# Kernel optimization log

Hardware: AMD Instinct MI355X
Metric: run time of the kernel (lower is better)

Reference implementation:

```python
import jax, jax.numpy as jnp
import numpy as np

NEURAL_DIM = 512
N_UNITS = 512
N_DAYS = 24
N_CLASSES = 41
N_LAYERS = 5
PATCH = 14
STRIDE = 4
MEMORY_SIZE = 256
IN0 = NEURAL_DIM * PATCH  # 7168, layer-0 input after patch concat


def _expm(M):
    """Matrix exponential via scaling-and-squaring + Taylor (float64 numpy)."""
    nrm = np.linalg.norm(M, 1)
    s = max(0, int(np.ceil(np.log2(nrm))) + 4) if nrm > 0 else 0
    Ms = M / (2.0 ** s)
    n = M.shape[0]
    E = np.eye(n)
    term = np.eye(n)
    for k in range(1, 25):
        term = term @ Ms / k
        E = E + term
    for _ in range(s):
        E = E @ E
    return E


def _lmu_AB(m_size):
    # NOTE: the torch cell calls _compute_A_B(memory_size, B.shape[0]), so the
    # effective theta used for discretization is memory_size itself.
    theta = float(m_size)
    q = np.arange(m_size, dtype=np.float64)
    R = ((2.0 * q + 1.0) / theta).reshape(-1, 1)
    i, j = np.meshgrid(q, q, indexing='ij')
    A = R * np.where(i < j, -1.0, (-1.0) ** (i - j + 1))
    Bc = R * ((-1.0) ** q).reshape(-1, 1)
    # zero-order hold discretization with dt=1: expm([[A,B],[0,0]])
    aug = np.zeros((m_size + 1, m_size + 1))
    aug[:m_size, :m_size] = A
    aug[:m_size, m_size:] = Bc
    E = _expm(aug)
    return (jnp.asarray(E[:m_size, :m_size], dtype=jnp.float32),
            jnp.asarray(E[:m_size, m_size:], dtype=jnp.float32))


A_MAT, B_MAT = _lmu_AB(MEMORY_SIZE)  # [M,M], [M,1]


def setup_inputs() -> dict:
    key = jax.random.key(0)
    ks = jax.random.split(key, 20)

    def rn(k, shape, scale):
        return jax.random.normal(k, shape, dtype=jnp.float32) * scale

    inp = {
        'x': jax.random.normal(ks[0], (32, 1024, NEURAL_DIM), dtype=jnp.float32),
        'day_idx': jax.random.randint(ks[1], (32,), 0, N_DAYS),
        # day-specific input layers (init: identity + zero bias; perturb slightly)
        'day_W': jnp.broadcast_to(jnp.eye(NEURAL_DIM, dtype=jnp.float32), (N_DAYS, NEURAL_DIM, NEURAL_DIM)) + rn(ks[2], (N_DAYS, NEURAL_DIM, NEURAL_DIM), 0.01),
        'day_b': rn(ks[3], (N_DAYS, 1, NEURAL_DIM), 0.01),
        # layer 0 (input 7168)
        'e_x0': rn(ks[4], (1, IN0), 1.0 / np.sqrt(IN0)),
        'W_x0': rn(ks[5], (N_UNITS, IN0), np.sqrt(2.0 / (IN0 + N_UNITS))),
        # layers 1..4 (input 512)
        'e_xr': rn(ks[6], (N_LAYERS - 1, 1, N_UNITS), 1.0 / np.sqrt(N_UNITS)),
        'W_xr': rn(ks[7], (N_LAYERS - 1, N_UNITS, N_UNITS), np.sqrt(1.0 / N_UNITS)),
        # shared-shape per-layer params (stacked over 5 layers)
        'e_h': rn(ks[8], (N_LAYERS, 1, N_UNITS), 1.0 / np.sqrt(N_UNITS)),
        'e_m': rn(ks[9], (N_LAYERS, 1, MEMORY_SIZE), 0.02),
        'W_h': rn(ks[10], (N_LAYERS, N_UNITS, N_UNITS), np.sqrt(1.0 / N_UNITS)),
        'W_m': rn(ks[11], (N_LAYERS, N_UNITS, MEMORY_SIZE), np.sqrt(2.0 / (MEMORY_SIZE + N_UNITS))),
        'h0': rn(ks[12], (N_LAYERS, 1, N_UNITS), 0.05),
        'm0': rn(ks[13], (N_LAYERS, 1, MEMORY_SIZE), 0.05),
        'out_W': rn(ks[14], (N_CLASSES, N_UNITS), np.sqrt(2.0 / (N_UNITS + N_CLASSES))),
        'out_b': jnp.zeros((N_CLASSES,), dtype=jnp.float32),
    }
    return inp


def _run_lmu_layer(seq, e_x, W_x, e_h, e_m, W_h, W_m, h_init, m_init):
    """seq: [B,T,in] -> [B,T,H] LMU recurrence."""
    # precompute input projections (the only big GEMMs) outside the scan
    xWx = jnp.einsum('bti,hi->bth', seq, W_x)   # [B,T,H]
    xex = jnp.einsum('bti,oi->bto', seq, e_x)   # [B,T,1]

    def step(carry, inp):
        h, m = carry
        xw, xe = inp
        u = xe + h @ e_h.T + m @ e_m.T          # [B,1]
        m = m @ A_MAT.T + u @ B_MAT.T           # [B,M]
        h = jnp.tanh(xw + h @ W_h.T + m @ W_m.T)
        return (h, m), h

    (_, _), hs = jax.lax.scan(step, (h_init, m_init),
                              (jnp.swapaxes(xWx, 0, 1), jnp.swapaxes(xex, 0, 1)))
    return jnp.swapaxes(hs, 0, 1)  # [B,T,H]


def reference(x, day_idx, day_W, day_b, e_x0, W_x0, e_xr, W_xr,
              e_h, e_m, W_h, W_m, h0, m0, out_W, out_b):
    B = x.shape[0]
    # day-specific linear + softsign
    h = jnp.einsum('btd,bdk->btk', x, day_W[day_idx]) + day_b[day_idx]
    h = h / (1.0 + jnp.abs(h))  # Softsign
    # patch concat: unfold time dim with window=PATCH, stride=STRIDE
    T = h.shape[1]
    Tp = (T - PATCH) // STRIDE + 1
    idx = jnp.arange(Tp)[:, None] * STRIDE + jnp.arange(PATCH)[None, :]
    h = h[:, idx, :].reshape(B, Tp, PATCH * NEURAL_DIM)  # [B,Tp,7168]

    bc = lambda v, d: jnp.broadcast_to(v, (B, d))
    seq = _run_lmu_layer(h, e_x0, W_x0, e_h[0], e_m[0], W_h[0], W_m[0],
                         bc(h0[0], N_UNITS), bc(m0[0], MEMORY_SIZE))
    for i in range(1, N_LAYERS):
        seq = _run_lmu_layer(seq, e_xr[i - 1], W_xr[i - 1], e_h[i], e_m[i],
                             W_h[i], W_m[i], bc(h0[i], N_UNITS), bc(m0[i], MEMORY_SIZE))
    logits = seq @ out_W.T + out_b  # [B,Tp,n_classes]
    return logits
```

## Files before the change

### kernel.cpp

```cpp
#include <hip/hip_runtime.h>
#include <hip/hip_fp16.h>

typedef _Float16 f16;
typedef _Float16 f16x8 __attribute__((ext_vector_type(8)));
typedef _Float16 f16x4 __attribute__((ext_vector_type(4)));
typedef float f32x4 __attribute__((ext_vector_type(4)));
typedef int int4v __attribute__((ext_vector_type(4)));

#define DI static __device__ __forceinline__

constexpr int N2 = 257 * 257;
#define LSTRIDE ((size_t)254 * 32 * 768)
#define HWREG_XCC_ID 63508
#define FSTRIDE 256

DI f32x4 mfma16(f16x8 a, f16x8 b, f32x4 c) {
  return __builtin_amdgcn_mfma_f32_16x16x32_f16(a, b, c, 0, 0, 0);
}
DI f16x8 ldg8(const f16* p) { return *reinterpret_cast<const f16x8*>(p); }
DI f16x8 cvt8(const float* s) {
  f16x8 v;
#pragma unroll
  for (int j = 0; j < 8; ++j) v[j] = (f16)s[j];
  return v;
}
DI double invfact(int k) {
  double f = 1.0;
  for (int i = 2; i <= k; ++i) f *= (double)i;
  return 1.0 / f;
}

DI void st_d_sc1(double* p, double v) {
  asm volatile("global_store_dwordx2 %0, %1, off sc1" :: "v"(p), "v"(v) : "memory");
}
DI void st_f_sc1(float* p, float v) {
  asm volatile("global_store_dword %0, %1, off sc1" :: "v"(p), "v"(v) : "memory");
}
DI void st_h_sc1(f16* p, f16 v) {
  asm volatile("global_store_short %0, %1, off sc1" :: "v"(p), "v"(v) : "memory");
}
DI void st_b_sc1(unsigned char* p, int v) {
  asm volatile("global_store_byte %0, %1, off sc1" :: "v"(p), "v"(v) : "memory");
}
DI void st8_sc1(f16* p, f16x4 v) {
  asm volatile("global_store_dwordx2 %0, %1, off sc1\n\ts_waitcnt vmcnt(0)"
               :: "v"(p), "v"(v) : "memory");
}
DI void st8_plain(f16* p, f16x4 v) {
  asm volatile("global_store_dwordx2 %0, %1, off\n\ts_waitcnt vmcnt(0)"
               :: "v"(p), "v"(v) : "memory");
}
DI void st8_fast(f16* p, f16x4 v) {
  asm volatile(
      "global_store_dwordx2 %0, %1, off\n\t"
      "global_store_dwordx2 %0, %1, off sc1\n\t"
      "s_waitcnt vmcnt(1)"
      :: "v"(p), "v"(v) : "memory");
}
DI void atomic_bump_l2(int* p) {
  int one = 1;
  asm volatile("global_atomic_add %0, %1, off" :: "v"(p), "v"(one) : "memory");
}
DI int atomic_read_l2(int* p) {
  int v, zero = 0;
  asm volatile("global_atomic_add %0, %1, %2, off sc0\n\ts_waitcnt vmcnt(0)"
               : "=v"(v) : "v"(p), "v"(zero) : "memory");
  return v;
}
DI int ld_llc(const int* p) {
  return __hip_atomic_load(p, __ATOMIC_RELAXED, __HIP_MEMORY_SCOPE_AGENT);
}
DI void add_llc(int* p) {
  __hip_atomic_fetch_add(p, 1, __ATOMIC_RELAXED, __HIP_MEMORY_SCOPE_AGENT);
}
DI int fetchadd_llc(int* p) {
  return __hip_atomic_fetch_add(p, 1, __ATOMIC_RELAXED, __HIP_MEMORY_SCOPE_AGENT);
}
DI void drain_vm() { asm volatile("s_waitcnt vmcnt(0)" ::: "memory"); }
DI void membar() {
  __builtin_amdgcn_sched_barrier(0);
  asm volatile("" ::: "memory");
}
DI bool l16ok(int4v a) {
  return a.x == 0x01010101 && a.y == 0x01010101 && a.z == 0x01010101 && a.w == 0x01010101;
}
DI int4v ld16_sc1(const int* p) {
  int4v b;
  asm volatile("global_load_dwordx4 %0, %1, off sc1\n\ts_waitcnt vmcnt(0)"
               : "=v"(b) : "v"(p) : "memory");
  return b;
}
template <bool HASP>
DI void poll_slow(const int* fl, const int* pl) {
  for (int it = 0; it < (1 << 14); ++it) {
    int4v b, c;
    asm volatile(
        "global_load_dwordx4 %0, %2, off sc1\n\t"
        "global_load_dwordx4 %1, %3, off sc1\n\t"
        "s_waitcnt vmcnt(0)"
        : "=&v"(b), "=&v"(c)
        : "v"(fl), "v"(pl) : "memory");
    bool prv = HASP ? l16ok(c) : true;
    if (l16ok(b) & prv) return;
    __builtin_amdgcn_s_sleep(1);
  }
}
DI float tanh_fast(float x) {
  x = fminf(9.f, fmaxf(-9.f, x));
  float e = __expf(2.f * x);
  return __fdividef(e - 1.f, e + 1.f);
}

DI void gridbar_nf(int* bar, int nwg) {
  drain_vm();
  __syncthreads();
  if (threadIdx.x == 0) {
    int g = ld_llc(bar + 1);
    int old = __hip_atomic_fetch_add(bar, 1, __ATOMIC_RELAXED, __HIP_MEMORY_SCOPE_AGENT);
    if (old == nwg - 1) {
      __hip_atomic_store(bar, 0, __ATOMIC_RELAXED, __HIP_MEMORY_SCOPE_AGENT);
      add_llc(bar + 1);
    } else {
      for (int it = 0; it < (1 << 14) && ld_llc(bar + 1) == g; ++it)
        __builtin_amdgcn_s_sleep(1);
    }
  }
  __syncthreads();
}

DI void mm257(double* __restrict__ D, const double* __restrict__ A, const double* __restrict__ Bm,
              int fj, const double* __restrict__ T1, const double* __restrict__ T2,
              const double* __restrict__ T3, int gtid, int nth) {
  double c0 = 0, c1 = 0, c2 = 0, c3 = 0;
  if (fj >= 0) {
    c0 = invfact(4 * fj); c1 = invfact(4 * fj + 1);
    c2 = invfact(4 * fj + 2); c3 = invfact(4 * fj + 3);
  }
  for (int e = gtid; e < N2; e += nth) {
    int i = e / 257, j = e - i * 257;
    const double* ar = A + (size_t)i * 257;
    const double* bc = Bm + j;
    double s0 = 0, s1 = 0, s2 = 0, s3 = 0;
    for (int k = 0; k < 256; k += 4) {
      s0 = fma(ar[k], bc[(size_t)k * 257], s0);
      s1 = fma(ar[k + 1], bc[(size_t)(k + 1) * 257], s1);
      s2 = fma(ar[k + 2], bc[(size_t)(k + 2) * 257], s2);
      s3 = fma(ar[k + 3], bc[(size_t)(k + 3) * 257], s3);
    }
    double s = ((s0 + s1) + (s2 + s3)) + ar[256] * bc[(size_t)256 * 257];
    if (fj >= 0) s += c0 * ((i == j) ? 1.0 : 0.0) + c1 * T1[e] + c2 * T2[e] + c3 * T3[e];
    st_d_sc1(D + e, s);
  }
}

__global__ __launch_bounds__(256) void k_setup(
    const float* __restrict__ dayW, const float* __restrict__ ex0, const float* __restrict__ Wx0,
    const float* __restrict__ exr, const float* __restrict__ Wxr,
    const float* __restrict__ eh, const float* __restrict__ em,
    const float* __restrict__ Wh, const float* __restrict__ Wm, const float* __restrict__ outW,
    double* __restrict__ X, float* __restrict__ w1f, float* __restrict__ AWt,
    float* __restrict__ btf, f16* __restrict__ gbuf, f16* __restrict__ wxcat,
    f16* __restrict__ outw, f16* __restrict__ dayWt, int* __restrict__ bar) {
  const int gtid = blockIdx.x * 256 + threadIdx.x;
  const int nth = 128 * 256;
  double* Ms = X;
  double* M2 = X + N2;
  double* M3 = X + 2 * N2;
  double* M4 = X + 3 * N2;
  double* H = X + 4 * N2;
  double* S = X + 11 * N2;

  for (int e = gtid; e < N2; e += nth) {
    int i = e / 257, j = e - i * 257;
    double v = 0.0;
    if (i < 256) {
      double R = (2.0 * i + 1.0) / 256.0;
      if (j < 256) v = R * ((i < j) ? -1.0 : (((i - j) & 1) ? 1.0 : -1.0));
      else v = R * ((i & 1) ? -1.0 : 1.0);
    }
    st_d_sc1(Ms + e, v / 64.0);
  }
  for (int e = gtid; e < 576 * 896; e += nth) {
    int n = e / 896, kc = (e - n * 896) * 8;
    f16x8 v;
    if (n < 512) v = cvt8(Wx0 + (size_t)n * 7168 + kc);
    else if (n == 512) v = cvt8(ex0 + kc);
    else {
#pragma unroll
      for (int j = 0; j < 8; ++j) v[j] = (f16)0.f;
    }
    *reinterpret_cast<f16x8*>(wxcat + (size_t)n * 7168 + kc) = v;
  }
  for (int e = gtid; e < 48 * 64; e += nth) {
    int n = e / 64, kc = (e - n * 64) * 8;
    f16x8 v;
    if (n < 41) v = cvt8(outW + (size_t)n * 512 + kc);
    else {
#pragma unroll
      for (int j = 0; j < 8; ++j) v[j] = (f16)0.f;
    }
    *reinterpret_cast<f16x8*>(outw + (size_t)n * 512 + kc) = v;
  }
  {
    __shared__ float tile[64][65];
    for (int tt = blockIdx.x; tt < 24 * 64; tt += 128) {
      int D = tt >> 6; int r = tt & 63; int kb = (r >> 3) * 64; int nb = (r & 7) * 64;
      __syncthreads();
      for (int q = 0; q < 16; ++q) {
        int idx = threadIdx.x + q * 256; int kk = idx >> 6; int nn = idx & 63;
        tile[kk][nn] = dayW[(size_t)D * 262144 + (size_t)(kb + kk) * 512 + nb + nn];
      }
      __syncthreads();
      for (int q = 0; q < 2; ++q) {
        int cidx = threadIdx.x + q * 256; int nn = cidx >> 3; int kc = (cidx & 7) * 8;
        f16x8 v;
#pragma unroll
        for (int jj = 0; jj < 8; ++jj) v[jj] = (f16)tile[kc + jj][nn];
        *reinterpret_cast<f16x8*>(dayWt + (size_t)D * 262144 + (size_t)(nb + nn) * 512 + kb + kc) = v;
      }
    }
    __syncthreads();
  }
  gridbar_nf(bar, 128);

  mm257(M2, Ms, Ms, -1, Ms, Ms, Ms, gtid, nth); gridbar_nf(bar, 128);
  mm257(M3, M2, Ms, -1, Ms, Ms, Ms, gtid, nth); gridbar_nf(bar, 128);
  mm257(M4, M2, M2, -1, Ms, Ms, Ms, gtid, nth);
  for (int e = gtid; e < N2; e += nth) {
    int i = e / 257, j = e - i * 257;
    st_d_sc1(H + e, (i == j) ? invfact(24) : 0.0);
  }
  gridbar_nf(bar, 128);
  for (int k = 0; k < 6; ++k) {
    mm257(H + (size_t)(k + 1) * N2, H + (size_t)k * N2, M4, 5 - k, Ms, M2, M3, gtid, nth);
    gridbar_nf(bar, 128);
  }
  {
    const double* Ssrc = H + (size_t)6 * N2;
    for (int k = 0; k < 6; ++k) {
      mm257(S + (size_t)k * N2, Ssrc, Ssrc, -1, Ms, Ms, Ms, gtid, nth);
      gridbar_nf(bar, 128);
      Ssrc = S + (size_t)k * N2;
    }
  }
  const double* E = S + (size_t)5 * N2;

  for (int e = gtid; e < 256; e += nth) st_f_sc1(btf + e, (float)E[(size_t)e * 257 + 256]);
  for (int e = gtid; e < 5 * 512; e += nth) {
    int l = e / 512, n = e - l * 512;
    const float* wm = Wm + ((size_t)l * 512 + n) * 256;
    float s = 0.f;
    for (int j = 0; j < 256; ++j) s += (float)E[(size_t)j * 257 + 256] * wm[j];
    st_f_sc1(w1f + e, s);
  }
  for (int e = gtid; e < 5 * 512 * 256; e += nth) {
    int l = e / (512 * 256); int r = e - l * 512 * 256; int n = r >> 8; int i = r & 255;
    const double* Ec = E + i;
    const float* wm = Wm + ((size_t)l * 512 + n) * 256;
    float s0 = 0, s1 = 0, s2 = 0, s3 = 0;
    for (int j = 0; j < 256; j += 4) {
      s0 += (float)Ec[(size_t)j * 257] * wm[j];
      s1 += (float)Ec[(size_t)(j + 1) * 257] * wm[j + 1];
      s2 += (float)Ec[(size_t)(j + 2) * 257] * wm[j + 2];
      s3 += (float)Ec[(size_t)(j + 3) * 257] * wm[j + 3];
    }
    st_f_sc1(AWt + e, (s0 + s1) + (s2 + s3));
  }
  gridbar_nf(bar, 128);

  for (int e = gtid; e < 5 * 768 * 160; e += nth) {
    int l = e / (768 * 160); int r = e - l * 768 * 160; int n = r / 160; int k = (r - n * 160) * 8;
    if (l == 0 && k >= 768) continue;
    f16x8 v;
    if (n < 512) {
      float w1n = w1f[l * 512 + n];
      if (k < 512) {
        const float* a = Wh + ((size_t)l * 512 + n) * 512 + k;
        const float* b = eh + (size_t)l * 512 + k;
#pragma unroll
        for (int jj = 0; jj < 8; ++jj) v[jj] = (f16)(a[jj] + b[jj] * w1n);
      } else if (k < 768) {
        int i = k - 512;
        const float* a = AWt + ((size_t)l * 512 + n) * 256 + i;
        const float* b = em + (size_t)l * 256 + i;
#pragma unroll
        for (int jj = 0; jj < 8; ++jj) v[jj] = (f16)(a[jj] + b[jj] * w1n);
      } else {
        int d = k - 768;
        const float* a = Wxr + ((size_t)(l - 1) * 512 + n) * 512 + d;
        const float* b = exr + (size_t)(l - 1) * 512 + d;
#pragma unroll
        for (int jj = 0; jj < 8; ++jj) v[jj] = (f16)(a[jj] + b[jj] * w1n);
      }
    } else {
      int jm = n - 512;
      float btn = btf[jm];
      if (k < 512) {
        const float* b = eh + (size_t)l * 512 + k;
#pragma unroll
        for (int jj = 0; jj < 8; ++jj) v[jj] = (f16)(b[jj] * btn);
      } else if (k < 768) {
        int i = k - 512;
        const double* a = E + (size_t)jm * 257 + i;
        const float* b = em + (size_t)l * 256 + i;
#pragma unroll
        for (int jj = 0; jj < 8; ++jj) v[jj] = (f16)((float)a[jj] + b[jj] * btn);
      } else {
        int d = k - 768;
        const float* b = exr + (size_t)(l - 1) * 512 + d;
#pragma unroll
        for (int jj = 0; jj < 8; ++jj) v[jj] = (f16)(b[jj] * btn);
      }
    }
    *reinterpret_cast<f16x8*>(gbuf + ((size_t)l * 768 + n) * 1280 + k) = v;
  }
}

__global__ __launch_bounds__(256) void k_day(const float* __restrict__ x,
    const int* __restrict__ dayIdx, const float* __restrict__ dayb,
    const f16* __restrict__ dayWt, f16* __restrict__ h1) {
  __shared__ f16 As[64][40];
  __shared__ f16 Bs[256][40];
  const int bid = blockIdx.x;
  const int b = bid >> 5; const int r = bid & 31;
  const int t0 = (r >> 1) * 64; const int n0 = (r & 1) * 256;
  const int D = dayIdx[b];
  const int tid = threadIdx.x, lane = tid & 63, w = tid >> 6, q4 = lane >> 4;
  const float* xb = x + ((size_t)b * 1024 + t0) * 512;
  const f16* Wt = dayWt + (size_t)D * 262144 + (size_t)n0 * 512;
  f32x4 acc[16];
#pragma unroll
  for (int i = 0; i < 16; ++i) acc[i] = (f32x4){0.f, 0.f, 0.f, 0.f};
  for (int kt = 0; kt < 16; ++kt) {
    const int k0 = kt * 32;
    __syncthreads();
    { int row = tid >> 2, c8 = (tid & 3) * 8;
      *reinterpret_cast<f16x8*>(&As[row][c8]) = cvt8(xb + (size_t)row * 512 + k0 + c8); }
    for (int q = 0; q < 4; ++q) {
      int idx = tid + q * 256; int row = idx >> 2; int c8 = (idx & 3) * 8;
      *reinterpret_cast<f16x8*>(&Bs[row][c8]) = ldg8(Wt + (size_t)row * 512 + k0 + c8);
    }
    __syncthreads();
    f16x8 a = *reinterpret_cast<const f16x8*>(&As[w * 16 + (lane & 15)][q4 * 8]);
#pragma unroll
    for (int nt2 = 0; nt2 < 16; ++nt2) {
      f16x8 bb = *reinterpret_cast<const f16x8*>(&Bs[nt2 * 16 + (lane & 15)][q4 * 8]);
      acc[nt2] = mfma16(a, bb, acc[nt2]);
    }
  }
#pragma unroll
  for (int nt2 = 0; nt2 < 16; ++nt2) {
    int n = n0 + nt2 * 16 + (lane & 15);
    float db = dayb[(size_t)D * 512 + n];
#pragma unroll
    for (int i = 0; i < 4; ++i) {
      int t = t0 + w * 16 + q4 * 4 + i;
      float v = acc[nt2][i] + db;
      v = v / (1.f + fabsf(v));
      h1[((size_t)b * 1024 + t) * 512 + n] = (f16)v;
    }
  }
}

__global__ __launch_bounds__(256) void k_xw0(const f16* __restrict__ h1,
    const f16* __restrict__ wxcat, float* __restrict__ xw0) {
  __shared__ f16 As[128][40];
  __shared__ f16 Bs[96][40];
  const int bid = blockIdx.x;
  const int mt = bid / 6; const int nb = bid - mt * 6;
  const int m0 = mt * 128; const int n0 = nb * 96;
  const int tid = threadIdx.x, lane = tid & 63, w = tid >> 6, q4 = lane >> 4;
  f32x4 acc[2][6];
#pragma unroll
  for (int a = 0; a < 2; ++a)
#pragma unroll
    for (int b = 0; b < 6; ++b) acc[a][b] = (f32x4){0.f, 0.f, 0.f, 0.f};
  for (int kt = 0; kt < 224; ++kt) {
    const int k0 = kt * 32; const int p = k0 >> 9; const int kd = k0 & 511;
    __syncthreads();
    for (int q = 0; q < 2; ++q) {
      int idx = tid + q * 256; int row = idx >> 2; int c8 = (idx & 3) * 8;
      int m = m0 + row; int b = m >> 8; int tp = m & 255; if (tp > 252) tp = 252;
      *reinterpret_cast<f16x8*>(&As[row][c8]) =
          ldg8(h1 + ((size_t)b * 1024 + (size_t)tp * 4 + p) * 512 + kd + c8);
    }
    for (int q = 0; q < 2; ++q) {
      int idx = tid + q * 256;
      if (idx < 384) {
        int row = idx >> 2; int c8 = (idx & 3) * 8;
        *reinterpret_cast<f16x8*>(&Bs[row][c8]) =
            ldg8(wxcat + (size_t)(n0 + row) * 7168 + k0 + c8);
      }
    }
    __syncthreads();
#pragma unroll
    for (int mb = 0; mb < 2; ++mb) {
      f16x8 a = *reinterpret_cast<const f16x8*>(&As[w * 32 + mb * 16 + (lane & 15)][q4 * 8]);
#pragma unroll
      for (int nt2 = 0; nt2 < 6; ++nt2) {
        f16x8 bb = *reinterpret_cast<const f16x8*>(&Bs[nt2 * 16 + (lane & 15)][q4 * 8]);
        acc[mb][nt2] = mfma16(a, bb, acc[mb][nt2]);
      }
    }
  }
#pragma unroll
  for (int mb = 0; mb < 2; ++mb)
#pragma unroll
    for (int nt2 = 0; nt2 < 6; ++nt2)
#pragma unroll
      for (int i = 0; i < 4; ++i) {
        int m = m0 + w * 32 + mb * 16 + q4 * 4 + i;
        int n = n0 + nt2 * 16 + (lane & 15);
        xw0[(size_t)m * 576 + n] = acc[mb][nt2][i];
      }
}

template <int KK, bool FAST>
DI void rec_run(int l, int c, int tid, const f16* __restrict__ gbuf, f16* __restrict__ sbuf,
                const float* __restrict__ xw0, const float* __restrict__ w1f,
                const float* __restrict__ btf, const float* __restrict__ h0,
                const float* __restrict__ m0, char* fastL, unsigned char* fastX,
                unsigned char* slowF, f16* bflds, f16* smtile) {
  const int lane = tid & 63, w = tid >> 6;
  const int mb = w / 3, nt = w % 3;
  const int nbase = c * 48 + nt * 16;
  const int ncol = nbase + (lane & 15);
  const int q4 = lane >> 4;

  for (int r = tid; r < 32 * 48; r += 384) {
    int row = r / 48; int col = c * 48 + (r - row * 48);
    float v = (col < 512) ? h0[(size_t)l * 512 + col] : m0[(size_t)l * 256 + col - 512];
    f16* p = sbuf + (size_t)l * LSTRIDE + (size_t)row * 768 + col;
    if (FAST) *p = (f16)v;
    else st_h_sc1(p, (f16)v);
  }

  const f16* gb = gbuf + ((size_t)l * 768 + ncol) * 1280 + (size_t)q4 * 8;
  constexpr int NREG = (KK > 32) ? 32 : KK;
  f16x8 bf[NREG];
#pragma unroll
  for (int kk = 0; kk < NREG; ++kk) bf[kk] = ldg8(gb + (size_t)kk * 32);
  if (KK == 40) {
#pragma unroll
    for (int kk = 32; kk < 40; ++kk) {
      f16x8 v = ldg8(gb + (size_t)kk * 32);
      *reinterpret_cast<f16x8*>(bflds + ((size_t)(w * 8 + (kk - 32)) * 64 + lane) * 8) = v;
    }
  }
  float w1n = 0.f, btn = 0.f;
  if (KK == 24) {
    if (ncol < 512) w1n = w1f[ncol];
    else btn = btf[ncol - 512];
  }
  drain_vm();
  __syncthreads();
  if (tid == 0) {
    if (FAST) {
      atomic_bump_l2((int*)(fastL + (size_t)l * 4096));
      st_b_sc1(fastX + (size_t)(l * 256) * 16 + c, 1);
    } else {
      st_b_sc1(slowF + (size_t)(l * FSTRIDE) * 16 + c, 1);
    }
  }

  int pready = 0;
  int lwin = 64, lfails = 0;

  for (int t = 0; t < 253; ++t) {
    float xadd[4];
    if (KK == 24) {
#pragma unroll
      for (int i = 0; i < 4; ++i) {
        const int brow = mb * 16 + q4 * 4 + i;
        const float* xr = xw0 + ((size_t)brow * 256 + t) * 576;
        float xe = xr[512];
        xadd[i] = (ncol < 512) ? (xr[ncol] + xe * w1n) : (xe * btn);
      }
    }
    if (tid == 0) {
      if (FAST) {
        if (l > 0 && pready <= t) {
          int la = t + 4; if (la > 253) la = 253;
          const int* p1 = (const int*)(fastX + (size_t)((l - 1) * 256 + t + 1) * 16);
          const int* p2 = (const int*)(fastX + (size_t)((l - 1) * 256 + la) * 16);
          for (int it = 0; it < (1 << 14); ++it) {
            int4v a, b;
            asm volatile(
                "global_load_dwordx4 %0, %2, off sc1\n\t"
                "global_load_dwordx4 %1, %3, off sc1\n\t"
                "s_waitcnt vmcnt(0)"
                : "=&v"(a), "=&v"(b) : "v"(p1), "v"(p2) : "memory");
            if (l16ok(b)) { pready = la; break; }
            if (l16ok(a)) { pready = t + 1; break; }
            __builtin_amdgcn_s_sleep(1);
          }
        }
        int* cl = (int*)(fastL + (size_t)l * 4096 + (size_t)t * 16);
        bool got = false;
        for (int it = 0; it < lwin; ++it) {
          if (atomic_read_l2(cl) >= 16) { got = true; break; }
          __builtin_amdgcn_s_sleep(1);
        }
        if (!got) {
          if (++lfails >= 3) lwin = 4;
          const int* fx = (const int*)(fastX + (size_t)(l * 256 + t) * 16);
          for (int j = 0; j < (1 << 14); ++j) {
            if (atomic_read_l2(cl) >= 16) break;
            if (l16ok(ld16_sc1(fx))) break;
            __builtin_amdgcn_s_sleep(1);
          }
        }
      } else {
        const int* fl = (const int*)(slowF + (size_t)(l * FSTRIDE + t) * 16);
        const int* pl = (l > 0) ? (const int*)(slowF + (size_t)((l - 1) * FSTRIDE + t + 1) * 16) : fl;
        if (l > 0) poll_slow<true>(fl, pl);
        else poll_slow<false>(fl, pl);
      }
    }
    __builtin_amdgcn_s_barrier();
    membar();

    const int arow = mb * 16 + (lane & 15);
    const f16* s0 = sbuf + (size_t)l * LSTRIDE + ((size_t)t * 32 + arow) * 768 + (size_t)q4 * 8;
    f32x4 acc = {0.f, 0.f, 0.f, 0.f};
#pragma unroll
    for (int kk = 0; kk < 24; ++kk) acc = mfma16(ldg8(s0 + (size_t)kk * 32), bf[kk < NREG ? kk : 0], acc);
    if (KK == 40) {
      const f16* s1 = sbuf + (size_t)(l - 1) * LSTRIDE + ((size_t)(t + 1) * 32 + arow) * 768 + (size_t)q4 * 8;
#pragma unroll
      for (int kk = 24; kk < 32; ++kk) acc = mfma16(ldg8(s1 + (size_t)(kk - 24) * 32), bf[kk < NREG ? kk : 0], acc);
#pragma unroll
      for (int kk = 32; kk < 40; ++kk) {
        f16x8 bb = *reinterpret_cast<const f16x8*>(bflds + ((size_t)(w * 8 + (kk - 32)) * 64 + lane) * 8);
        acc = mfma16(ldg8(s1 + (size_t)(kk - 24) * 32), bb, acc);
      }
    }

    const int scol = nt * 16 + (lane & 15);
#pragma unroll
    for (int i = 0; i < 4; ++i) {
      float v = acc[i];
      if (KK == 24) v += xadd[i];
      if (ncol < 512) v = tanh_fast(v);
      smtile[(mb * 16 + q4 * 4 + i) * 48 + scol] = (f16)v;
    }
    __syncthreads();
    {
      int row = tid / 12; int c4 = (tid - row * 12) * 4;
      f16x4 v4 = *reinterpret_cast<const f16x4*>(smtile + row * 48 + c4);
      f16* dst = sbuf + (size_t)l * LSTRIDE + ((size_t)(t + 1) * 32 + row) * 768 + c * 48 + c4;
      if (!FAST) st8_sc1(dst, v4);
      else if (l < 4) st8_fast(dst, v4);
      else st8_plain(dst, v4);
    }
    __builtin_amdgcn_s_barrier();
    if (FAST) {
      if (tid == 0) atomic_bump_l2((int*)(fastL + (size_t)l * 4096 + (size_t)(t + 1) * 16));
      if (l < 4) drain_vm();
      __builtin_amdgcn_s_barrier();
      if (tid == 0) st_b_sc1(fastX + (size_t)(l * 256 + t + 1) * 16 + c, 1);
    } else {
      if (tid == 0) st_b_sc1(slowF + (size_t)(l * FSTRIDE + t + 1) * 16 + c, 1);
    }
  }
}

__global__ __launch_bounds__(384, 2) void k_rec(const f16* __restrict__ gbuf, f16* __restrict__ sbuf,
    const float* __restrict__ xw0, const float* __restrict__ w1f,
    const float* __restrict__ btf, const float* __restrict__ h0,
    const float* __restrict__ m0, char* __restrict__ fastL,
    unsigned char* __restrict__ fastX, unsigned char* __restrict__ slowF,
    int* __restrict__ xcdcnt, int* __restrict__ globalcnt, int* __restrict__ verdict) {
  __shared__ f16 bflds[6 * 8 * 64 * 8];
  __shared__ f16 smtile[32 * 48];
  __shared__ int sh[4];

  if (threadIdx.x == 0) {
    unsigned xcd = ((unsigned)__builtin_amdgcn_s_getreg(HWREG_XCC_ID)) & 7u;
    int pt = fetchadd_llc(xcdcnt + xcd);
    drain_vm();
    int gt = fetchadd_llc(globalcnt);
    if (gt == 255) {
      int ok = 1;
      for (int i = 0; i < 5; ++i)
        if (ld_llc(xcdcnt + i) < 16) ok = 0;
      __hip_atomic_store(verdict, ok ? 1 : 2, __ATOMIC_RELAXED, __HIP_MEMORY_SCOPE_AGENT);
    }
    int v = 0;
    for (int it = 0; it < (1 << 17); ++it) {
      v = ld_llc(verdict);
      if (v) break;
      __builtin_amdgcn_s_sleep(4);
    }
    if (v == 0) v = 2;
    int L = -1, C = 0;
    if (v == 1) {
      if (xcd < 5 && pt < 16) { L = (int)xcd; C = pt; }
    } else {
      if (gt < 80) { L = gt >> 4; C = gt & 15; }
    }
    sh[0] = L; sh[1] = C; sh[2] = (L >= 0); sh[3] = (v == 1);
  }
  __syncthreads();
  if (!sh[2]) return;
  const int l = sh[0], c = sh[1];
  const bool fast = (sh[3] != 0);

  if (fast) {
    if (l == 0) rec_run<24, true>(0, c, threadIdx.x, gbuf, sbuf, xw0, w1f, btf, h0, m0, fastL, fastX, slowF, bflds, smtile);
    else        rec_run<40, true>(l, c, threadIdx.x, gbuf, sbuf, xw0, w1f, btf, h0, m0, fastL, fastX, slowF, bflds, smtile);
  } else {
    if (l == 0) rec_run<24, false>(0, c, threadIdx.x, gbuf, sbuf, xw0, w1f, btf, h0, m0, fastL, fastX, slowF, bflds, smtile);
    else        rec_run<40, false>(l, c, threadIdx.x, gbuf, sbuf, xw0, w1f, btf, h0, m0, fastL, fastX, slowF, bflds, smtile);
  }
}

__global__ __launch_bounds__(256) void k_out(const f16* __restrict__ sbuf4,
    const f16* __restrict__ outw, const float* __restrict__ outb, float* __restrict__ out) {
  const int bid = blockIdx.x; const int b = bid >> 2; const int tp0 = (bid & 3) * 64;
  const int tid = threadIdx.x, lane = tid & 63, w = tid >> 6, q4 = lane >> 4;
  f32x4 acc[3];
#pragma unroll
  for (int i = 0; i < 3; ++i) acc[i] = (f32x4){0.f, 0.f, 0.f, 0.f};
  int tq = tp0 + w * 16 + (lane & 15) + 1;
  const int tau = tq > 253 ? 253 : tq;
  const f16* arow = sbuf4 + ((size_t)tau * 32 + b) * 768 + (size_t)q4 * 8;
#pragma unroll
  for (int kk = 0; kk < 16; ++kk) {
    f16x8 a = ldg8(arow + (size_t)kk * 32);
#pragma unroll
    for (int nt2 = 0; nt2 < 3; ++nt2) {
      f16x8 bb = ldg8(outw + (size_t)(nt2 * 16 + (lane & 15)) * 512 + kk * 32 + q4 * 8);
      acc[nt2] = mfma16(a, bb, acc[nt2]);
    }
  }
#pragma unroll
  for (int nt2 = 0; nt2 < 3; ++nt2) {
    int cc = nt2 * 16 + (lane & 15);
    if (cc < 41) {
      float ob = outb[cc];
#pragma unroll
      for (int i = 0; i < 4; ++i) {
        int tp = tp0 + w * 16 + q4 * 4 + i;
        if (tp < 253) out[((size_t)b * 253 + tp) * 41 + cc] = acc[nt2][i] + ob;
      }
    }
  }
}

extern "C" void kernel_launch(void* const* d_in, const int* in_sizes, int n_in,
                              void* d_out, int out_size, void* d_ws, size_t ws_size,
                              hipStream_t stream) {
  const float* x      = (const float*)d_in[0];
  const int*   dayIdx = (const int*)d_in[1];
  const float* day_W  = (const float*)d_in[2];
  const float* day_b  = (const float*)d_in[3];
  const float* e_x0   = (const float*)d_in[4];
  const float* W_x0   = (const float*)d_in[5];
  const float* e_xr   = (const float*)d_in[6];
  const float* W_xr   = (const float*)d_in[7];
  const float* e_h    = (const float*)d_in[8];
  const float* e_m    = (const float*)d_in[9];
  const float* W_h    = (const float*)d_in[10];
  const float* W_m    = (const float*)d_in[11];
  const float* h0     = (const float*)d_in[12];
  const float* m0     = (const float*)d_in[13];
  const float* out_W  = (const float*)d_in[14];
  const float* out_b  = (const float*)d_in[15];
  float* outp = (float*)d_out;

  char* w = (char*)d_ws;
  size_t o = 0;
  auto al = [&](size_t n) { void* p = w + o; o = (o + n + 255) & ~(size_t)255; return p; };

  char*  flags = (char*) al(65536);
  f16*   gbuf  = (f16*)  al((size_t)5 * 768 * 1280 * 2);
  f16*   outw  = (f16*)  al((size_t)48 * 512 * 2);
  float* xw0   = (float*)al((size_t)8192 * 576 * 4);
  float* w1f   = (float*)al((size_t)5 * 512 * 4);
  float* btf   = (float*)al(256 * 4);

  const size_t XB    = ((size_t)17 * N2 * 8 + 255) & ~(size_t)255;
  const size_t AWTB  = ((size_t)5 * 512 * 256 * 4 + 255) & ~(size_t)255;
  const size_t DAYB  = ((size_t)24 * 512 * 512 * 2 + 255) & ~(size_t)255;
  const size_t WXB   = ((size_t)576 * 7168 * 2 + 255) & ~(size_t)255;
  const size_t H1B   = ((size_t)32 * 1024 * 512 * 2 + 255) & ~(size_t)255;
  const size_t SBUFB = (size_t)5 * LSTRIDE * 2;
  size_t ovb = XB + AWTB + DAYB + WXB + H1B;
  if (SBUFB > ovb) ovb = SBUFB;
  char* ov = (char*)al(ovb);
  double* X     = (double*)ov;
  float*  AWt   = (float*)(ov + XB);
  f16*    dayWt = (f16*)(ov + XB + AWTB);
  f16*    wxcat = (f16*)(ov + XB + AWTB + DAYB);
  f16*    h1    = (f16*)(ov + XB + AWTB + DAYB + WXB);
  f16*    sbuf  = (f16*)ov;

  if (o > ws_size) return;
  (void)in_sizes; (void)n_in; (void)out_size;

  hipMemsetAsync(flags, 0, 65536, stream);
  k_setup<<<128, 256, 0, stream>>>(day_W, e_x0, W_x0, e_xr, W_xr, e_h, e_m, W_h, W_m,
                                   out_W, X, w1f, AWt, btf, gbuf, wxcat, outw, dayWt,
                                   (int*)(flags + 61504));
  k_day<<<1024, 256, 0, stream>>>(x, dayIdx, day_b, dayWt, h1);
  k_xw0<<<384, 256, 0, stream>>>(h1, wxcat, xw0);
  k_rec<<<256, 384, 0, stream>>>(gbuf, sbuf, xw0, w1f, btf, h0, m0,
                                 flags, (unsigned char*)(flags + 20480),
                                 (unsigned char*)(flags + 40960),
                                 (int*)(flags + 61440), (int*)(flags + 61472),
                                 (int*)(flags + 61476));
  k_out<<<128, 256, 0, stream>>>(sbuf + (size_t)4 * LSTRIDE, outw, out_b, outp);
}
```

Before: 4.166 ms.

## Add per-XCD byte flag array for fast-path step sync and block mm257 by four columns

Adds a new fastP byte-flag array that each producer block writes with a plain store, and consumers poll it with a 16-byte sc0 load instead of reading an L2 atomic counter. The atomic counter and the sc1 flags stay as fallbacks. This aims to cut the latency of the per-timestep cross-block handoff in the recurrent kernel. It also restructures the setup matrix multiply so each thread computes four adjacent output columns, reusing each A element for four FMAs. The flag region grows and its offsets move. There is a risk that plain and sc0 accesses may not be coherent across XCDs, which would make the fallback path run more often.

New measurement: 5.812 ms. 39.5% more time.

```diff
diff --git a/kernel.cpp b/kernel.cpp
--- a/kernel.cpp
+++ b/kernel.cpp
@@ -38,6 +38,9 @@
 }
 DI void st_h_sc1(f16* p, f16 v) {
   asm volatile("global_store_short %0, %1, off sc1" :: "v"(p), "v"(v) : "memory");
+}
+DI void st_b_plain(unsigned char* p, int v) {
+  asm volatile("global_store_byte %0, %1, off" :: "v"(p), "v"(v) : "memory");
 }
 DI void st_b_sc1(unsigned char* p, int v) {
   asm volatile("global_store_byte %0, %1, off sc1" :: "v"(p), "v"(v) : "memory");
@@ -83,6 +86,12 @@
 }
 DI bool l16ok(int4v a) {
   return a.x == 0x01010101 && a.y == 0x01010101 && a.z == 0x01010101 && a.w == 0x01010101;
+}
+DI int4v ld16_sc0(const int* p) {
+  int4v b;
+  asm volatile("global_load_dwordx4 %0, %1, off sc0\n\ts_waitcnt vmcnt(0)"
+               : "=v"(b) : "v"(p) : "memory");
+  return b;
 }
 DI int4v ld16_sc1(const int* p) {
   int4v b;
@@ -136,20 +145,36 @@
     c0 = invfact(4 * fj); c1 = invfact(4 * fj + 1);
     c2 = invfact(4 * fj + 2); c3 = invfact(4 * fj + 3);
   }
-  for (int e = gtid; e < N2; e += nth) {
-    int i = e / 257, j = e - i * 257;
+  const int NB = 257 * 65;
+  for (int e = gtid; e < NB; e += nth) {
+    int i = e / 65, jb = e - i * 65;
+    int j0 = jb * 4;
     const double* ar = A + (size_t)i * 257;
-    const double* bc = Bm + j;
-    double s0 = 0, s1 = 0, s2 = 0, s3 = 0;
-    for (int k = 0; k < 256; k += 4) {
-      s0 = fma(ar[k], bc[(size_t)k * 257], s0);
-      s1 = fma(ar[k + 1], bc[(size_t)(k + 1) * 257], s1);
-      s2 = fma(ar[k + 2], bc[(size_t)(k + 2) * 257], s2);
-      s3 = fma(ar[k + 3], bc[(size_t)(k + 3) * 257], s3);
-    }
-    double s = ((s0 + s1) + (s2 + s3)) + ar[256] * bc[(size_t)256 * 257];
-    if (fj >= 0) s += c0 * ((i == j) ? 1.0 : 0.0) + c1 * T1[e] + c2 * T2[e] + c3 * T3[e];
-    st_d_sc1(D + e, s);
+    if (j0 < 256) {
+      const double* bc = Bm + j0;
+      double s0 = 0, s1 = 0, s2 = 0, s3 = 0;
+      for (int k = 0; k < 257; ++k) {
+        double a = ar[k];
+        const double* br = bc + (size_t)k * 257;
+        s0 = fma(a, br[0], s0); s1 = fma(a, br[1], s1);
+        s2 = fma(a, br[2], s2); s3 = fma(a, br[3], s3);
+      }
+      double sv[4] = {s0, s1, s2, s3};
+#pragma unroll
+      for (int jj = 0; jj < 4; ++jj) {
+        int j = j0 + jj; int idx = i * 257 + j;
+        double s = sv[jj];
+        if (fj >= 0) s += c0 * ((i == j) ? 1.0 : 0.0) + c1 * T1[idx] + c2 * T2[idx] + c3 * T3[idx];
+        st_d_sc1(D + idx, s);
+      }
+    } else {
+      const double* bc = Bm + 256;
+      double s = 0;
+      for (int k = 0; k < 257; ++k) s = fma(ar[k], bc[(size_t)k * 257], s);
+      int idx = i * 257 + 256;
+      if (fj >= 0) s += c0 * ((i == 256) ? 1.0 : 0.0) + c1 * T1[idx] + c2 * T2[idx] + c3 * T3[idx];
+      st_d_sc1(D + idx, s);
+    }
   }
 }
 
@@ -420,7 +445,7 @@
                 const float* __restrict__ xw0, const float* __restrict__ w1f,
                 const float* __restrict__ btf, const float* __restrict__ h0,
                 const float* __restrict__ m0, char* fastL, unsigned char* fastX,
-                unsigned char* slowF, f16* bflds, f16* smtile) {
+                unsigned char* fastP, unsigned char* slowF, f16* bflds, f16* smtile) {
   const int lane = tid & 63, w = tid >> 6;
   const int mb = w / 3, nt = w % 3;
   const int nbase = c * 48 + nt * 16;
@@ -456,6 +481,7 @@
   __syncthreads();
   if (tid == 0) {
     if (FAST) {
+      st_b_plain(fastP + (size_t)(l * 256) * 16 + c, 1);
       atomic_bump_l2((int*)(fastL + (size_t)l * 4096));
       st_b_sc1(fastX + (size_t)(l * 256) * 16 + c, 1);
     } else {
@@ -495,16 +521,20 @@
             __builtin_amdgcn_s_sleep(1);
           }
         }
-        int* cl = (int*)(fastL + (size_t)l * 4096 + (size_t)t * 16);
+        const int* fp = (const int*)(fastP + (size_t)(l * 256 + t) * 16);
         bool got = false;
         for (int it = 0; it < lwin; ++it) {
-          if (atomic_read_l2(cl) >= 16) { got = true; break; }
+          if (l16ok(ld16_sc0(fp))) { got = true; break; }
           __builtin_amdgcn_s_sleep(1);
         }
-        if (!got) {
+        if (got) {
+          lfails = 0; lwin = 64;
+        } else {
           if (++lfails >= 3) lwin = 4;
+          int* cl = (int*)(fastL + (size_t)l * 4096 + (size_t)t * 16);
           const int* fx = (const int*)(fastX + (size_t)(l * 256 + t) * 16);
           for (int j = 0; j < (1 << 14); ++j) {
+            if (l16ok(ld16_sc0(fp))) break;
             if (atomic_read_l2(cl) >= 16) break;
             if (l16ok(ld16_sc1(fx))) break;
             __builtin_amdgcn_s_sleep(1);
@@ -555,7 +585,10 @@
     }
     __builtin_amdgcn_s_barrier();
     if (FAST) {
-      if (tid == 0) atomic_bump_l2((int*)(fastL + (size_t)l * 4096 + (size_t)(t + 1) * 16));
+      if (tid == 0) {
+        st_b_plain(fastP + (size_t)(l * 256 + t + 1) * 16 + c, 1);
+        atomic_bump_l2((int*)(fastL + (size_t)l * 4096 + (size_t)(t + 1) * 16));
+      }
       if (l < 4) drain_vm();
       __builtin_amdgcn_s_barrier();
       if (tid == 0) st_b_sc1(fastX + (size_t)(l * 256 + t + 1) * 16 + c, 1);
@@ -569,7 +602,8 @@
     const float* __restrict__ xw0, const float* __restrict__ w1f,
     const float* __restrict__ btf, const float* __restrict__ h0,
     const float* __restrict__ m0, char* __restrict__ fastL,
-    unsigned char* __restrict__ fastX, unsigned char* __restrict__ slowF,
+    unsigned char* __restrict__ fastX, unsigned char* __restrict__ fastP,
+    unsigned char* __restrict__ slowF,
     int* __restrict__ xcdcnt, int* __restrict__ globalcnt, int* __restrict__ verdict) {
   __shared__ f16 bflds[6 * 8 * 64 * 8];
   __shared__ f16 smtile[32 * 48];
@@ -607,11 +641,11 @@
   const bool fast = (sh[3] != 0);
 
   if (fast) {
-    if (l == 0) rec_run<24, true>(0, c, threadIdx.x, gbuf, sbuf, xw0, w1f, btf, h0, m0, fastL, fastX, slowF, bflds, smtile);
-    else        rec_run<40, true>(l, c, threadIdx.x, gbuf, sbuf, xw0, w1f, btf, h0, m0, fastL, fastX, slowF, bflds, smtile);
+    if (l == 0) rec_run<24, true>(0, c, threadIdx.x, gbuf, sbuf, xw0, w1f, btf, h0, m0, fastL, fastX, fastP, slowF, bflds, smtile);
+    else        rec_run<40, true>(l, c, threadIdx.x, gbuf, sbuf, xw0, w1f, btf, h0, m0, fastL, fastX, fastP, slowF, bflds, smtile);
   } else {
-    if (l == 0) rec_run<24, false>(0, c, threadIdx.x, gbuf, sbuf, xw0, w1f, btf, h0, m0, fastL, fastX, slowF, bflds, smtile);
-    else        rec_run<40, false>(l, c, threadIdx.x, gbuf, sbuf, xw0, w1f, btf, h0, m0, fastL, fastX, slowF, bflds, smtile);
+    if (l == 0) rec_run<24, false>(0, c, threadIdx.x, gbuf, sbuf, xw0, w1f, btf, h0, m0, fastL, fastX, fastP, slowF, bflds, smtile);
+    else        rec_run<40, false>(l, c, threadIdx.x, gbuf, sbuf, xw0, w1f, btf, h0, m0, fastL, fastX, fastP, slowF, bflds, smtile);
   }
 }
 
@@ -673,7 +707,7 @@
   size_t o = 0;
   auto al = [&](size_t n) { void* p = w + o; o = (o + n + 255) & ~(size_t)255; return p; };
 
-  char*  flags = (char*) al(65536);
+  char*  flags = (char*) al(131072);
   f16*   gbuf  = (f16*)  al((size_t)5 * 768 * 1280 * 2);
   f16*   outw  = (f16*)  al((size_t)48 * 512 * 2);
   float* xw0   = (float*)al((size_t)8192 * 576 * 4);
@@ -699,16 +733,17 @@
   if (o > ws_size) return;
   (void)in_sizes; (void)n_in; (void)out_size;
 
-  hipMemsetAsync(flags, 0, 65536, stream);
+  hipMemsetAsync(flags, 0, 131072, stream);
   k_setup<<<128, 256, 0, stream>>>(day_W, e_x0, W_x0, e_xr, W_xr, e_h, e_m, W_h, W_m,
                                    out_W, X, w1f, AWt, btf, gbuf, wxcat, outw, dayWt,
-                                   (int*)(flags + 61504));
+                                   (int*)(flags + 82176));
   k_day<<<1024, 256, 0, stream>>>(x, dayIdx, day_b, dayWt, h1);
   k_xw0<<<384, 256, 0, stream>>>(h1, wxcat, xw0);
   k_rec<<<256, 384, 0, stream>>>(gbuf, sbuf, xw0, w1f, btf, h0, m0,
                                  flags, (unsigned char*)(flags + 20480),
+                                 (unsigned char*)(flags + 61440),
                                  (unsigned char*)(flags + 40960),
-                                 (int*)(flags + 61440), (int*)(flags + 61472),
-                                 (int*)(flags + 61476));
+                                 (int*)(flags + 81920), (int*)(flags + 81952),
+                                 (int*)(flags + 81956));
   k_out<<<128, 256, 0, stream>>>(sbuf + (size_t)4 * LSTRIDE, outw, out_b, outp);
 }
```
